# Performance work log

Hardware: AMD Instinct MI355X
Metric: run time of the kernel (lower is better)

Reference implementation:

```python
import jax, jax.numpy as jnp
import numpy as np

N_NODES, N_EDGES = 16384, 8192
IN_CH, HID_CH = 256, 256
ALPHA, BETA = -1.5, -0.5


def setup_inputs() -> dict:
    key = jax.random.key(0)
    k1, k2, k3, k4, k5, k6 = jax.random.split(key, 6)
    x_0 = jax.random.normal(k1, (N_NODES, IN_CH), dtype=jnp.float32)
    # binary incidence matrix (n_nodes, n_edges)
    incidence_1 = jax.random.randint(k2, (N_NODES, N_EDGES), 0, 2).astype(jnp.float32)
    # conv weights (torch Conv: x @ W then neighborhood @ .)
    W0 = jax.random.normal(k3, (IN_CH, HID_CH), dtype=jnp.float32) * 0.02
    W1 = jax.random.normal(k4, (HID_CH, HID_CH), dtype=jnp.float32) * 0.02
    # xavier_uniform biases of shape (1, hidden)
    gain = 1.414
    bound = gain * np.sqrt(6.0 / (1 + HID_CH)) * np.sqrt(3.0) / np.sqrt(3.0)  # xavier bound = gain*sqrt(6/(fan_in+fan_out))
    bound = gain * np.sqrt(6.0 / (1 + HID_CH))
    bias_0_to_1 = jax.random.uniform(k5, (1, HID_CH), minval=-bound, maxval=bound, dtype=jnp.float32)
    bias_1_to_0 = jax.random.uniform(k6, (1, HID_CH), minval=-bound, maxval=bound, dtype=jnp.float32)
    return {"x_0": x_0, "incidence_1": incidence_1, "W0": W0, "W1": W1,
            "bias_0_to_1": bias_0_to_1, "bias_1_to_0": bias_1_to_0}


def _normalize_incidence(B1):
    # edge/node cardinalities raised to alpha/beta
    edge_card = jnp.sum(B1, axis=0) ** ALPHA          # (n_edges,)
    node_card = jnp.sum(B1, axis=1) ** BETA           # (n_nodes,)
    mask = (B1 > 0).astype(B1.dtype)
    d0_inv = 1.0 / (mask @ edge_card)                 # (n_nodes,) per-node sum of incident edge_card
    d1_inv = 1.0 / (mask.T @ node_card)               # (n_edges,) per-edge sum of member node_card
    # B1_norm = D0_left^-1 @ B1 @ diag(edge_card)
    B1_norm = d0_inv[:, None] * B1 * edge_card[None, :]
    # B1T_norm = D1_left^-1 @ B1^T @ diag(node_card)
    B1T_norm = d1_inv[:, None] * B1.T * node_card[None, :]
    return B1_norm, B1T_norm


def reference(x_0, incidence_1, W0, W1, bias_0_to_1, bias_1_to_0):
    B1_norm, B1T_norm = _normalize_incidence(incidence_1)
    # node -> edge conv: x_1 = B1T_norm @ (x_0 @ W0) + b01
    x_1 = B1T_norm @ (x_0 @ W0) + bias_0_to_1        # (n_edges, hid)
    # edge -> node conv: x_0 = B1_norm @ (x_1 @ W1) + b10
    x_0_out = B1_norm @ (x_1 @ W1) + bias_1_to_0     # (n_nodes, hid)
    return jax.nn.relu(x_0_out), jax.nn.relu(x_1)
```

## Files before the change

### kernel.cpp

```cpp
#include <hip/hip_runtime.h>
#include <stdint.h>

#define NN 16384
#define NE 8192
#define CH 256
#define MM1_SPLIT 8
#define MM2_SPLIT 4

typedef __attribute__((ext_vector_type(8))) short bf16x8;
typedef __attribute__((ext_vector_type(4))) float f32x4;

__device__ __forceinline__ unsigned short f2bf(float f) {
  unsigned u = __float_as_uint(f);
  u += 0x7FFFu + ((u >> 16) & 1u);
  return (unsigned short)(u >> 16);
}
__device__ __forceinline__ unsigned pack_trunc2(float a, float b) {
  return (__float_as_uint(b) & 0xFFFF0000u) | (__float_as_uint(a) >> 16);
}
__device__ __forceinline__ void async_copy16(const void* gptr, void* lptr) {
  __builtin_amdgcn_global_load_lds((const __attribute__((address_space(1))) unsigned int*)gptr,
                                   (__attribute__((address_space(3))) unsigned int*)lptr,
                                   16, 0, 0);
}

__global__ void k0_transpose_w(const float* __restrict__ W0, const float* __restrict__ W1,
                               unsigned short* __restrict__ W0T, unsigned short* __restrict__ W1T) {
  const float* W = blockIdx.y ? W1 : W0;
  unsigned short* WT = blockIdx.y ? W1T : W0T;
  int n = blockIdx.x;
  int k = threadIdx.x;
  WT[n * CH + k] = f2bf(W[k * CH + n]);
}

__global__ void k1_node_card(const float* __restrict__ B1, float* __restrict__ node_card) {
  int n = blockIdx.x;
  const float4* row = (const float4*)(B1 + (size_t)n * NE);
  float s = 0.f;
#pragma unroll
  for (int j = 0; j < 8; ++j) {
    float4 v = row[threadIdx.x + j * 256];
    s += v.x + v.y + v.z + v.w;
  }
  __shared__ float red[4];
#pragma unroll
  for (int off = 32; off; off >>= 1) s += __shfl_down(s, off, 64);
  if ((threadIdx.x & 63) == 0) red[threadIdx.x >> 6] = s;
  __syncthreads();
  if (threadIdx.x == 0) {
    float t = red[0] + red[1] + red[2] + red[3];
    node_card[n] = rsqrtf(t);
  }
}

__global__ __launch_bounds__(256) void k2_y0(const float* __restrict__ X0,
                                             const unsigned short* __restrict__ W0T,
                                             const float* __restrict__ node_card,
                                             unsigned short* __restrict__ y0sT) {
  __shared__ unsigned short a_lds[64 * 32];
  __shared__ unsigned short b_lds[256 * 32];
  const int tid = threadIdx.x;
  const int wave = tid >> 6, lane = tid & 63;
  const int quad = lane >> 4, l15 = lane & 15;
  const int m0 = blockIdx.x * 64;
  const int ar = tid >> 3, ac = (tid & 7) * 4;

  f32x4 acc[4][4];
  const f32x4 fz = {0.f, 0.f, 0.f, 0.f};
#pragma unroll
  for (int i = 0; i < 4; ++i)
#pragma unroll
    for (int j = 0; j < 4; ++j) acc[i][j] = fz;

  for (int k0 = 0; k0 < CH; k0 += 32) {
    __syncthreads();
#pragma unroll
    for (int p = 0; p < 2; ++p) {
      float4 v = *(const float4*)(X0 + (size_t)(m0 + ar + p * 32) * CH + k0 + ac);
      uint2 w;
      w.x = ((unsigned)f2bf(v.x)) | ((unsigned)f2bf(v.y) << 16);
      w.y = ((unsigned)f2bf(v.z)) | ((unsigned)f2bf(v.w) << 16);
      *(uint2*)&a_lds[(ar + p * 32) * 32 + ac] = w;
    }
#pragma unroll
    for (int i = 0; i < 4; ++i) {
      int rowbase = wave * 64 + i * 16;
      const unsigned short* g = W0T + (size_t)(rowbase + (lane >> 2)) * CH + k0 + (lane & 3) * 8;
      async_copy16(g, &b_lds[rowbase * 32]);
    }
    __syncthreads();
    bf16x8 af[4];
#pragma unroll
    for (int i = 0; i < 4; ++i)
      af[i] = *(const bf16x8*)&a_lds[(i * 16 + l15) * 32 + quad * 8];
#pragma unroll
    for (int j = 0; j < 4; ++j) {
      bf16x8 bfr = *(const bf16x8*)&b_lds[(wave * 64 + j * 16 + l15) * 32 + quad * 8];
#pragma unroll
      for (int i = 0; i < 4; ++i)
        acc[i][j] = __builtin_amdgcn_mfma_f32_16x16x32_bf16(af[i], bfr, acc[i][j], 0, 0, 0);
    }
  }
#pragma unroll
  for (int i = 0; i < 4; ++i) {
    int row4 = m0 + i * 16 + quad * 4;
    float4 nc = *(const float4*)(node_card + row4);
#pragma unroll
    for (int j = 0; j < 4; ++j) {
      int col = wave * 64 + j * 16 + l15;
      f32x4 v = acc[i][j];
      ushort4 o;
      o.x = f2bf(v[0] * nc.x);
      o.y = f2bf(v[1] * nc.y);
      o.z = f2bf(v[2] * nc.z);
      o.w = f2bf(v[3] * nc.w);
      *(ushort4*)&y0sT[(size_t)col * NN + row4] = o;
    }
  }
}

__global__ void k2b_aux(const float* __restrict__ node_card, unsigned short* __restrict__ y0sT) {
  int n = blockIdx.x * 256 + threadIdx.x;
  y0sT[(size_t)256 * NN + n] = f2bf(node_card[n]);
  y0sT[(size_t)257 * NN + n] = 0x3F80;
#pragma unroll
  for (int r = 258; r < 272; ++r) y0sT[(size_t)r * NN + n] = 0;
}

__global__ __launch_bounds__(256) void mm1_kernel(const float* __restrict__ B1,
                                                  const unsigned short* __restrict__ y0sT,
                                                  float* __restrict__ mm1p,
                                                  float* __restrict__ auxD,
                                                  float* __restrict__ auxC) {
  __shared__ unsigned short a_lds[64 * 40];
  __shared__ unsigned short b_lds[272 * 32];
  const int tid = threadIdx.x;
  const int wave = tid >> 6, lane = tid & 63;
  const int quad = lane >> 4, l15 = lane & 15;
  const int m0 = blockIdx.x * 64;
  const int sp = blockIdx.y;
  const int KS = NN / MM1_SPLIT;
  const int kbase = sp * KS;

  const int am4 = (tid & 15) * 4;
  const int anp = tid >> 4;
  const int ajb = anp >> 2, alow = anp & 3;

  f32x4 acc[4][4];
  f32x4 acc5[4];
  const f32x4 fz = {0.f, 0.f, 0.f, 0.f};
#pragma unroll
  for (int i = 0; i < 4; ++i) {
    acc5[i] = fz;
#pragma unroll
    for (int j = 0; j < 4; ++j) acc[i][j] = fz;
  }

  const float* agp = B1 + (size_t)(kbase + 2 * anp) * NE + m0 + am4;
  float4 va = *(const float4*)(agp);
  float4 vb = *(const float4*)(agp + NE);

  for (int kk = 0; kk < KS; kk += 32) {
    const int k0 = kbase + kk;
    __syncthreads();
    {
#pragma unroll
      for (int i = 0; i < 4; ++i) {
        int m = am4 + i;
        unsigned w = pack_trunc2(((const float*)&va)[i], ((const float*)&vb)[i]);
        int jbs = ajb ^ ((m >> 4) & 3);
        *(unsigned*)&a_lds[m * 40 + (jbs * 4 + alow) * 2] = w;
      }
    }
#pragma unroll
    for (int i = 0; i < 4; ++i) {
      int rowbase = wave * 64 + i * 16;
      const unsigned short* g = y0sT + (size_t)(rowbase + (lane >> 2)) * NN + k0 + (lane & 3) * 8;
      async_copy16(g, &b_lds[rowbase * 32]);
    }
    if (wave == 3) {
      const unsigned short* g = y0sT + (size_t)(256 + (lane >> 2)) * NN + k0 + (lane & 3) * 8;
      async_copy16(g, &b_lds[256 * 32]);
    }
    __syncthreads();
    if (kk + 32 < KS) {
      agp += (size_t)32 * NE;
      va = *(const float4*)(agp);
      vb = *(const float4*)(agp + NE);
    }
    bf16x8 af[4];
#pragma unroll
    for (int i = 0; i < 4; ++i) {
      int m = i * 16 + l15;
      int jbs = quad ^ ((m >> 4) & 3);
      af[i] = *(const bf16x8*)&a_lds[m * 40 + jbs * 8];
    }
#pragma unroll
    for (int j = 0; j < 4; ++j) {
      bf16x8 bfr = *(const bf16x8*)&b_lds[(wave * 64 + j * 16 + l15) * 32 + quad * 8];
#pragma unroll
      for (int i = 0; i < 4; ++i)
        acc[i][j] = __builtin_amdgcn_mfma_f32_16x16x32_bf16(af[i], bfr, acc[i][j], 0, 0, 0);
    }
    if (wave == 3) {
      bf16x8 bfr = *(const bf16x8*)&b_lds[(256 + l15) * 32 + quad * 8];
#pragma unroll
      for (int i = 0; i < 4; ++i)
        acc5[i] = __builtin_amdgcn_mfma_f32_16x16x32_bf16(af[i], bfr, acc5[i], 0, 0, 0);
    }
  }
  float* outp = mm1p + (size_t)sp * NE * CH;
#pragma unroll
  for (int i = 0; i < 4; ++i) {
    int row4 = m0 + i * 16 + quad * 4;
#pragma unroll
    for (int j = 0; j < 4; ++j) {
      int col = wave * 64 + j * 16 + l15;
#pragma unroll
      for (int r = 0; r < 4; ++r) outp[(size_t)(row4 + r) * CH + col] = acc[i][j][r];
    }
  }
  if (wave == 3 && l15 < 2) {
    float* dst = (l15 == 0 ? auxD : auxC) + (size_t)sp * NE;
#pragma unroll
    for (int i = 0; i < 4; ++i) {
      int row4 = m0 + i * 16 + quad * 4;
#pragma unroll
      for (int r = 0; r < 4; ++r) dst[row4 + r] = acc5[i][r];
    }
  }
}

__global__ void k3_edge_final(const float* __restrict__ mm1p, const float* __restrict__ auxD,
                              const float* __restrict__ auxC, const float* __restrict__ b01,
                              float* __restrict__ out1, unsigned short* __restrict__ x1bf,
                              float* __restrict__ edge_card) {
  int e = blockIdx.x, c = threadIdx.x;
  float ds = 0.f, p = 0.f;
#pragma unroll
  for (int sp = 0; sp < MM1_SPLIT; ++sp) {
    ds += auxD[(size_t)sp * NE + e];
    p += mm1p[(size_t)sp * NE * CH + (size_t)e * CH + c];
  }
  float x1 = p / ds + b01[c];
  out1[(size_t)e * CH + c] = fmaxf(x1, 0.f);
  x1bf[(size_t)e * CH + c] = f2bf(x1);
  if (c == 0) {
    float cs = 0.f;
#pragma unroll
    for (int sp = 0; sp < MM1_SPLIT; ++sp) cs += auxC[(size_t)sp * NE + e];
    edge_card[e] = 1.0f / (cs * sqrtf(cs));
  }
}

__global__ __launch_bounds__(256) void k5_y1(const unsigned short* __restrict__ x1bf,
                                             const unsigned short* __restrict__ W1T,
                                             const float* __restrict__ edge_card,
                                             unsigned short* __restrict__ y1sT) {
  __shared__ unsigned short a_lds[64 * 32];
  __shared__ unsigned short b_lds[256 * 32];
  const int tid = threadIdx.x;
  const int wave = tid >> 6, lane = tid & 63;
  const int quad = lane >> 4, l15 = lane & 15;
  const int m0 = blockIdx.x * 64;

  f32x4 acc[4][4];
  const f32x4 fz = {0.f, 0.f, 0.f, 0.f};
#pragma unroll
  for (int i = 0; i < 4; ++i)
#pragma unroll
    for (int j = 0; j < 4; ++j) acc[i][j] = fz;

  for (int k0 = 0; k0 < CH; k0 += 32) {
    __syncthreads();
    {
      const unsigned short* g = x1bf + (size_t)(m0 + wave * 16 + (lane >> 2)) * CH + k0 + (lane & 3) * 8;
      async_copy16(g, &a_lds[(wave * 16) * 32]);
    }
#pragma unroll
    for (int i = 0; i < 4; ++i) {
      int rowbase = wave * 64 + i * 16;
      const unsigned short* g = W1T + (size_t)(rowbase + (lane >> 2)) * CH + k0 + (lane & 3) * 8;
      async_copy16(g, &b_lds[rowbase * 32]);
    }
    __syncthreads();
    bf16x8 af[4];
#pragma unroll
    for (int i = 0; i < 4; ++i)
      af[i] = *(const bf16x8*)&a_lds[(i * 16 + l15) * 32 + quad * 8];
#pragma unroll
    for (int j = 0; j < 4; ++j) {
      bf16x8 bfr = *(const bf16x8*)&b_lds[(wave * 64 + j * 16 + l15) * 32 + quad * 8];
#pragma unroll
      for (int i = 0; i < 4; ++i)
        acc[i][j] = __builtin_amdgcn_mfma_f32_16x16x32_bf16(af[i], bfr, acc[i][j], 0, 0, 0);
    }
  }
#pragma unroll
  for (int i = 0; i < 4; ++i) {
    int row4 = m0 + i * 16 + quad * 4;
    float4 ec = *(const float4*)(edge_card + row4);
#pragma unroll
    for (int j = 0; j < 4; ++j) {
      int col = wave * 64 + j * 16 + l15;
      f32x4 v = acc[i][j];
      ushort4 o;
      o.x = f2bf(v[0] * ec.x);
      o.y = f2bf(v[1] * ec.y);
      o.z = f2bf(v[2] * ec.z);
      o.w = f2bf(v[3] * ec.w);
      *(ushort4*)&y1sT[(size_t)col * NE + row4] = o;
    }
  }
}

__global__ void k5b_aux(const float* __restrict__ edge_card, unsigned short* __restrict__ y1sT) {
  int e = blockIdx.x * 256 + threadIdx.x;
  y1sT[(size_t)256 * NE + e] = f2bf(edge_card[e]);
#pragma unroll
  for (int r = 257; r < 272; ++r) y1sT[(size_t)r * NE + e] = 0;
}

__global__ __launch_bounds__(256) void mm2_kernel(const float* __restrict__ B1,
                                                  const unsigned short* __restrict__ y1sT,
                                                  float* __restrict__ mm2p,
                                                  float* __restrict__ d0p) {
  __shared__ unsigned short a_lds[64 * 40];
  __shared__ unsigned short b_lds[272 * 32];
  const int tid = threadIdx.x;
  const int wave = tid >> 6, lane = tid & 63;
  const int quad = lane >> 4, l15 = lane & 15;
  const int m0 = blockIdx.x * 64;
  const int sp = blockIdx.y;
  const int KS = NE / MM2_SPLIT;
  const int kbase = sp * KS;
  const int ar = tid >> 3, ac = (tid & 7) * 4;

  f32x4 acc[4][4];
  f32x4 acc5[4];
  const f32x4 fz = {0.f, 0.f, 0.f, 0.f};
#pragma unroll
  for (int i = 0; i < 4; ++i) {
    acc5[i] = fz;
#pragma unroll
    for (int j = 0; j < 4; ++j) acc[i][j] = fz;
  }

  const float* agp = B1 + (size_t)(m0 + ar) * NE + kbase + ac;
  float4 va = *(const float4*)(agp);
  float4 vb = *(const float4*)(agp + (size_t)32 * NE);

  for (int kk = 0; kk < KS; kk += 32) {
    const int k0 = kbase + kk;
    __syncthreads();
    {
      uint2 w0, w1;
      w0.x = pack_trunc2(va.x, va.y);
      w0.y = pack_trunc2(va.z, va.w);
      w1.x = pack_trunc2(vb.x, vb.y);
      w1.y = pack_trunc2(vb.z, vb.w);
      *(uint2*)&a_lds[ar * 40 + ac] = w0;
      *(uint2*)&a_lds[(ar + 32) * 40 + ac] = w1;
    }
#pragma unroll
    for (int i = 0; i < 4; ++i) {
      int rowbase = wave * 64 + i * 16;
      const unsigned short* g = y1sT + (size_t)(rowbase + (lane >> 2)) * NE + k0 + (lane & 3) * 8;
      async_copy16(g, &b_lds[rowbase * 32]);
    }
    if (wave == 3) {
      const unsigned short* g = y1sT + (size_t)(256 + (lane >> 2)) * NE + k0 + (lane & 3) * 8;
      async_copy16(g, &b_lds[256 * 32]);
    }
    __syncthreads();
    if (kk + 32 < KS) {
      agp += 32;
      va = *(const float4*)(agp);
      vb = *(const float4*)(agp + (size_t)32 * NE);
    }
    bf16x8 af[4];
#pragma unroll
    for (int i = 0; i < 4; ++i)
      af[i] = *(const bf16x8*)&a_lds[(i * 16 + l15) * 40 + quad * 8];
#pragma unroll
    for (int j = 0; j < 4; ++j) {
      bf16x8 bfr = *(const bf16x8*)&b_lds[(wave * 64 + j * 16 + l15) * 32 + quad * 8];
#pragma unroll
      for (int i = 0; i < 4; ++i)
        acc[i][j] = __builtin_amdgcn_mfma_f32_16x16x32_bf16(af[i], bfr, acc[i][j], 0, 0, 0);
    }
    if (wave == 3) {
      bf16x8 bfr = *(const bf16x8*)&b_lds[(256 + l15) * 32 + quad * 8];
#pragma unroll
      for (int i = 0; i < 4; ++i)
        acc5[i] = __builtin_amdgcn_mfma_f32_16x16x32_bf16(af[i], bfr, acc5[i], 0, 0, 0);
    }
  }
  float* outp = mm2p + (size_t)sp * NN * CH;
#pragma unroll
  for (int i = 0; i < 4; ++i) {
    int row4 = m0 + i * 16 + quad * 4;
#pragma unroll
    for (int j = 0; j < 4; ++j) {
      int col = wave * 64 + j * 16 + l15;
#pragma unroll
      for (int r = 0; r < 4; ++r) outp[(size_t)(row4 + r) * CH + col] = acc[i][j][r];
    }
  }
  if (wave == 3 && l15 == 0) {
#pragma unroll
    for (int i = 0; i < 4; ++i) {
      int row4 = m0 + i * 16 + quad * 4;
#pragma unroll
      for (int r = 0; r < 4; ++r) d0p[(size_t)sp * NN + row4 + r] = acc5[i][r];
    }
  }
}

__global__ void k6_node_final(const float* __restrict__ mm2p, const float* __restrict__ d0p,
                              const float* __restrict__ b10, float* __restrict__ out0) {
  int n = blockIdx.x, c = threadIdx.x;
  float s = 0.f, d = 0.f;
#pragma unroll
  for (int sp = 0; sp < MM2_SPLIT; ++sp) {
    s += mm2p[(size_t)sp * NN * CH + (size_t)n * CH + c];
    d += d0p[(size_t)sp * NN + n];
  }
  float v = s / d + b10[c];
  out0[(size_t)n * CH + c] = fmaxf(v, 0.f);
}

extern "C" void kernel_launch(void* const* d_in, const int* in_sizes, int n_in,
                              void* d_out, int out_size, void* d_ws, size_t ws_size,
                              hipStream_t stream) {
  const float* x0 = (const float*)d_in[0];
  const float* B1 = (const float*)d_in[1];
  const float* W0 = (const float*)d_in[2];
  const float* W1 = (const float*)d_in[3];
  const float* b01 = (const float*)d_in[4];
  const float* b10 = (const float*)d_in[5];
  float* out0 = (float*)d_out;
  float* out1 = out0 + (size_t)NN * CH;

  char* ws = (char*)d_ws;
  size_t off = 0;
  auto take = [&](size_t bytes) {
    void* p = ws + off;
    off += (bytes + 255) & ~(size_t)255;
    return p;
  };
  unsigned short* y0sT = (unsigned short*)take((size_t)272 * NN * 2);
  unsigned short* y1sT = (unsigned short*)take((size_t)272 * NE * 2);
  unsigned short* x1bf = (unsigned short*)take((size_t)NE * CH * 2);
  float* mm1p = (float*)take((size_t)MM1_SPLIT * NE * CH * 4);
  float* mm2p = mm1p;
  float* node_card = (float*)take((size_t)NN * 4);
  float* edge_card = (float*)take((size_t)NE * 4);
  float* auxD = (float*)take((size_t)MM1_SPLIT * NE * 4);
  float* auxC = (float*)take((size_t)MM1_SPLIT * NE * 4);
  float* d0p = (float*)take((size_t)MM2_SPLIT * NN * 4);
  unsigned short* W0T = (unsigned short*)take((size_t)CH * CH * 2);
  unsigned short* W1T = (unsigned short*)take((size_t)CH * CH * 2);
  (void)ws_size; (void)in_sizes; (void)n_in; (void)out_size;

  k0_transpose_w<<<dim3(256, 2), 256, 0, stream>>>(W0, W1, W0T, W1T);
  k1_node_card<<<NN, 256, 0, stream>>>(B1, node_card);
  k2_y0<<<NN / 64, 256, 0, stream>>>(x0, W0T, node_card, y0sT);
  k2b_aux<<<NN / 256, 256, 0, stream>>>(node_card, y0sT);
  mm1_kernel<<<dim3(NE / 64, MM1_SPLIT), 256, 0, stream>>>(B1, y0sT, mm1p, auxD, auxC);
  k3_edge_final<<<NE, 256, 0, stream>>>(mm1p, auxD, auxC, b01, out1, x1bf, edge_card);
  k5_y1<<<NE / 64, 256, 0, stream>>>(x1bf, W1T, edge_card, y1sT);
  k5b_aux<<<NE / 256, 256, 0, stream>>>(edge_card, y1sT);
  mm2_kernel<<<dim3(NN / 64, MM2_SPLIT), 256, 0, stream>>>(B1, y1sT, mm2p, d0p);
  k6_node_final<<<NN, 256, 0, stream>>>(mm2p, d0p, b10, out0);
}
```

Before: 1.147 ms.

## Convert incidence matrix to bf16 once and feed both GEMMs from it

The node-cardinality pass now also writes a bf16-truncated copy of the 512MB fp32 incidence matrix into workspace. Both big GEMMs then read that 256MB half-precision copy instead of re-reading the fp32 matrix, which halves their A-operand traffic and removes the in-loop float-to-bf16 packing. The GEMM grids are also flattened so consecutive blocks share the same output tile across K-splits. The cost is an extra 256MB write plus workspace space, which the two saved fp32 reads need to outweigh.

```diff
diff --git a/kernel.cpp b/kernel.cpp
--- a/kernel.cpp
+++ b/kernel.cpp
@@ -33,23 +33,29 @@
   WT[n * CH + k] = f2bf(W[k * CH + n]);
 }
 
-__global__ void k1_node_card(const float* __restrict__ B1, float* __restrict__ node_card) {
-  int n = blockIdx.x;
+__global__ void k1_prep(const float* __restrict__ B1, unsigned short* __restrict__ b1h,
+                        float* __restrict__ node_card) {
+  int n = blockIdx.x, t = threadIdx.x;
   const float4* row = (const float4*)(B1 + (size_t)n * NE);
+  unsigned short* orow = b1h + (size_t)n * NE;
   float s = 0.f;
 #pragma unroll
   for (int j = 0; j < 8; ++j) {
-    float4 v = row[threadIdx.x + j * 256];
+    float4 v = row[t + j * 256];
     s += v.x + v.y + v.z + v.w;
+    uint2 w;
+    w.x = pack_trunc2(v.x, v.y);
+    w.y = pack_trunc2(v.z, v.w);
+    *(uint2*)&orow[(t + j * 256) * 4] = w;
   }
   __shared__ float red[4];
 #pragma unroll
   for (int off = 32; off; off >>= 1) s += __shfl_down(s, off, 64);
-  if ((threadIdx.x & 63) == 0) red[threadIdx.x >> 6] = s;
+  if ((t & 63) == 0) red[t >> 6] = s;
   __syncthreads();
-  if (threadIdx.x == 0) {
-    float t = red[0] + red[1] + red[2] + red[3];
-    node_card[n] = rsqrtf(t);
+  if (t == 0) {
+    float tot = red[0] + red[1] + red[2] + red[3];
+    node_card[n] = rsqrtf(tot);
   }
 }
 
@@ -127,7 +133,7 @@
   for (int r = 258; r < 272; ++r) y0sT[(size_t)r * NN + n] = 0;
 }
 
-__global__ __launch_bounds__(256) void mm1_kernel(const float* __restrict__ B1,
+__global__ __launch_bounds__(256) void mm1_kernel(const unsigned short* __restrict__ b1h,
                                                   const unsigned short* __restrict__ y0sT,
                                                   float* __restrict__ mm1p,
                                                   float* __restrict__ auxD,
@@ -137,8 +143,9 @@
   const int tid = threadIdx.x;
   const int wave = tid >> 6, lane = tid & 63;
   const int quad = lane >> 4, l15 = lane & 15;
-  const int m0 = blockIdx.x * 64;
-  const int sp = blockIdx.y;
+  const int bid = blockIdx.x;
+  const int sp = bid & (MM1_SPLIT - 1);
+  const int m0 = (bid >> 3) * 64;
   const int KS = NN / MM1_SPLIT;
   const int kbase = sp * KS;
 
@@ -156,20 +163,24 @@
     for (int j = 0; j < 4; ++j) acc[i][j] = fz;
   }
 
-  const float* agp = B1 + (size_t)(kbase + 2 * anp) * NE + m0 + am4;
-  float4 va = *(const float4*)(agp);
-  float4 vb = *(const float4*)(agp + NE);
+  const unsigned short* agp = b1h + (size_t)(kbase + 2 * anp) * NE + m0 + am4;
+  uint2 va = *(const uint2*)agp;
+  uint2 vb = *(const uint2*)(agp + NE);
 
   for (int kk = 0; kk < KS; kk += 32) {
     const int k0 = kbase + kk;
     __syncthreads();
     {
+      unsigned w[4];
+      w[0] = (va.x & 0xFFFFu) | (vb.x << 16);
+      w[1] = (va.x >> 16) | (vb.x & 0xFFFF0000u);
+      w[2] = (va.y & 0xFFFFu) | (vb.y << 16);
+      w[3] = (va.y >> 16) | (vb.y & 0xFFFF0000u);
 #pragma unroll
       for (int i = 0; i < 4; ++i) {
         int m = am4 + i;
-        unsigned w = pack_trunc2(((const float*)&va)[i], ((const float*)&vb)[i]);
         int jbs = ajb ^ ((m >> 4) & 3);
-        *(unsigned*)&a_lds[m * 40 + (jbs * 4 + alow) * 2] = w;
+        *(unsigned*)&a_lds[m * 40 + (jbs * 4 + alow) * 2] = w[i];
       }
     }
 #pragma unroll
@@ -185,8 +196,8 @@
     __syncthreads();
     if (kk + 32 < KS) {
       agp += (size_t)32 * NE;
-      va = *(const float4*)(agp);
-      vb = *(const float4*)(agp + NE);
+      va = *(const uint2*)agp;
+      vb = *(const uint2*)(agp + NE);
     }
     bf16x8 af[4];
 #pragma unroll
@@ -321,20 +332,21 @@
   for (int r = 257; r < 272; ++r) y1sT[(size_t)r * NE + e] = 0;
 }
 
-__global__ __launch_bounds__(256) void mm2_kernel(const float* __restrict__ B1,
+__global__ __launch_bounds__(256) void mm2_kernel(const unsigned short* __restrict__ b1h,
                                                   const unsigned short* __restrict__ y1sT,
                                                   float* __restrict__ mm2p,
                                                   float* __restrict__ d0p) {
-  __shared__ unsigned short a_lds[64 * 40];
+  __shared__ unsigned short a_lds[64 * 32];
   __shared__ unsigned short b_lds[272 * 32];
   const int tid = threadIdx.x;
   const int wave = tid >> 6, lane = tid & 63;
   const int quad = lane >> 4, l15 = lane & 15;
-  const int m0 = blockIdx.x * 64;
-  const int sp = blockIdx.y;
+  const int bid = blockIdx.x;
+  const int sp = bid & (MM2_SPLIT - 1);
+  const int m0 = (bid >> 2) * 64;
   const int KS = NE / MM2_SPLIT;
   const int kbase = sp * KS;
-  const int ar = tid >> 3, ac = (tid & 7) * 4;
+  const int arow = tid >> 2, acol = (tid & 3) * 8;
 
   f32x4 acc[4][4];
   f32x4 acc5[4];
@@ -346,22 +358,13 @@
     for (int j = 0; j < 4; ++j) acc[i][j] = fz;
   }
 
-  const float* agp = B1 + (size_t)(m0 + ar) * NE + kbase + ac;
-  float4 va = *(const float4*)(agp);
-  float4 vb = *(const float4*)(agp + (size_t)32 * NE);
+  const unsigned short* agp = b1h + (size_t)(m0 + arow) * NE + kbase + acol;
+  uint4 va = *(const uint4*)agp;
 
   for (int kk = 0; kk < KS; kk += 32) {
     const int k0 = kbase + kk;
     __syncthreads();
-    {
-      uint2 w0, w1;
-      w0.x = pack_trunc2(va.x, va.y);
-      w0.y = pack_trunc2(va.z, va.w);
-      w1.x = pack_trunc2(vb.x, vb.y);
-      w1.y = pack_trunc2(vb.z, vb.w);
-      *(uint2*)&a_lds[ar * 40 + ac] = w0;
-      *(uint2*)&a_lds[(ar + 32) * 40 + ac] = w1;
-    }
+    *(uint4*)&a_lds[arow * 32 + acol] = va;
 #pragma unroll
     for (int i = 0; i < 4; ++i) {
       int rowbase = wave * 64 + i * 16;
@@ -375,13 +378,12 @@
     __syncthreads();
     if (kk + 32 < KS) {
       agp += 32;
-      va = *(const float4*)(agp);
-      vb = *(const float4*)(agp + (size_t)32 * NE);
+      va = *(const uint4*)agp;
     }
     bf16x8 af[4];
 #pragma unroll
     for (int i = 0; i < 4; ++i)
-      af[i] = *(const bf16x8*)&a_lds[(i * 16 + l15) * 40 + quad * 8];
+      af[i] = *(const bf16x8*)&a_lds[(i * 16 + l15) * 32 + quad * 8];
 #pragma unroll
     for (int j = 0; j < 4; ++j) {
       bf16x8 bfr = *(const bf16x8*)&b_lds[(wave * 64 + j * 16 + l15) * 32 + quad * 8];
@@ -449,6 +451,7 @@
     off += (bytes + 255) & ~(size_t)255;
     return p;
   };
+  unsigned short* b1h = (unsigned short*)take((size_t)NN * NE * 2);
   unsigned short* y0sT = (unsigned short*)take((size_t)272 * NN * 2);
   unsigned short* y1sT = (unsigned short*)take((size_t)272 * NE * 2);
   unsigned short* x1bf = (unsigned short*)take((size_t)NE * CH * 2);
@@ -464,13 +467,13 @@
   (void)ws_size; (void)in_sizes; (void)n_in; (void)out_size;
 
   k0_transpose_w<<<dim3(256, 2), 256, 0, stream>>>(W0, W1, W0T, W1T);
-  k1_node_card<<<NN, 256, 0, stream>>>(B1, node_card);
+  k1_prep<<<NN, 256, 0, stream>>>(B1, b1h, node_card);
   k2_y0<<<NN / 64, 256, 0, stream>>>(x0, W0T, node_card, y0sT);
   k2b_aux<<<NN / 256, 256, 0, stream>>>(node_card, y0sT);
-  mm1_kernel<<<dim3(NE / 64, MM1_SPLIT), 256, 0, stream>>>(B1, y0sT, mm1p, auxD, auxC);
+  mm1_kernel<<<(NE / 64) * MM1_SPLIT, 256, 0, stream>>>(b1h, y0sT, mm1p, auxD, auxC);
   k3_edge_final<<<NE, 256, 0, stream>>>(mm1p, auxD, auxC, b01, out1, x1bf, edge_card);
   k5_y1<<<NE / 64, 256, 0, stream>>>(x1bf, W1T, edge_card, y1sT);
   k5b_aux<<<NE / 256, 256, 0, stream>>>(edge_card, y1sT);
-  mm2_kernel<<<dim3(NN / 64, MM2_SPLIT), 256, 0, stream>>>(B1, y1sT, mm2p, d0p);
+  mm2_kernel<<<(NN / 64) * MM2_SPLIT, 256, 0, stream>>>(b1h, y1sT, mm2p, d0p);
   k6_node_final<<<NN, 256, 0, stream>>>(mm2p, d0p, b10, out0);
 }
```

Result: no change. 1.162 ms (+1.3%).
